# Kernel optimization log

Hardware: AMD Instinct MI355X
Metric: run time of the kernel (lower is better)

The kernel has to match this reference:

```python
import jax, jax.numpy as jnp
import numpy as np

L, D = 8192, 2048


def setup_inputs() -> dict:
    key = jax.random.key(0)
    kx, kA, kB, kC = jax.random.split(key, 4)
    x = jax.random.normal(kx, (L, D), dtype=jnp.float32)
    A = jax.random.normal(kA, (D,), dtype=jnp.float32)
    B = jax.random.normal(kB, (D,), dtype=jnp.float32)
    C = jax.random.normal(kC, (D,), dtype=jnp.float32)
    return {"x": x, "A": A, "B": B, "C": C}


def reference(x, A, B, C):
    # state_t = A * state_{t-1} + B * x_t ; y_t = tanh(C * state_t)
    Bx = B * x  # [L, D], precompute input injection

    def step(state, bx_t):
        state = A * state + bx_t
        return state, jnp.tanh(C * state)

    _, ys = jax.lax.scan(step, jnp.zeros((D,), dtype=x.dtype), Bx)
    return ys  # [L, D]
```

## Files before the change

kernel.cpp:

```cpp
#include <hip/hip_runtime.h>
#include <math.h>


#define LL 8192
#define DD 2048
#define CL 32
#define NC (LL / CL)
#define G4 (DD / 4)

typedef float f32x4 __attribute__((ext_vector_type(4)));

__device__ __forceinline__ float fast_tanh(float z)
{
    float e = __builtin_amdgcn_exp2f(z * 2.885390081777927f);
    return 1.0f - 2.0f * __builtin_amdgcn_rcpf(e + 1.0f);
}

__global__ __launch_bounds__(256) void mamba_p1(
    const float4* __restrict__ x4, const float4* __restrict__ A4,
    const float4* __restrict__ B4, float4* __restrict__ loc4)
{
    int lin   = blockIdx.x * 256 + threadIdx.x;
    int chunk = lin >> 9;
    int grp   = lin & (G4 - 1);

    float4 a = A4[grp];
    float4 b = B4[grp];
    float sx = 0.f, sy = 0.f, sz = 0.f, sw = 0.f;

    const float4* xp = x4 + (size_t)chunk * CL * G4 + grp;
    #pragma unroll
    for (int t0 = 0; t0 < CL; t0 += 16) {
        float4 v[16];
        #pragma unroll
        for (int k = 0; k < 16; ++k)
            v[k] = xp[(size_t)(t0 + k) * G4];
        #pragma unroll
        for (int k = 0; k < 16; ++k) {
            sx = fmaf(a.x, sx, b.x * v[k].x);
            sy = fmaf(a.y, sy, b.y * v[k].y);
            sz = fmaf(a.z, sz, b.z * v[k].z);
            sw = fmaf(a.w, sw, b.w * v[k].w);
        }
    }
    loc4[(size_t)chunk * G4 + grp] = make_float4(sx, sy, sz, sw);
}

__global__ __launch_bounds__(64) void mamba_p2(
    const float* __restrict__ A, const float* __restrict__ loc,
    float* __restrict__ car)
{
    int ch = blockIdx.x * 64 + threadIdx.x;
    float p = A[ch];
    #pragma unroll
    for (int i = 0; i < 5; ++i) p *= p;

    float c = 0.f;
    for (int c0 = 0; c0 < NC; c0 += 64) {
        float lv[64];
        #pragma unroll
        for (int k = 0; k < 64; ++k)
            lv[k] = loc[(size_t)(c0 + k) * DD + ch];
        #pragma unroll
        for (int k = 0; k < 64; ++k) {
            car[(size_t)(c0 + k) * DD + ch] = c;
            c = fmaf(p, c, lv[k]);
        }
    }
}

__global__ __launch_bounds__(256) void mamba_p3(
    const float4* __restrict__ x4, const float4* __restrict__ A4,
    const float4* __restrict__ B4, const float4* __restrict__ C4,
    const float4* __restrict__ car4, float4* __restrict__ y4)
{
    int lin   = blockIdx.x * 256 + threadIdx.x;
    int chunk = lin >> 9;
    int grp   = lin & (G4 - 1);

    float4 a = A4[grp];
    float4 b = B4[grp];
    float4 c = C4[grp];
    float4 s0 = car4[(size_t)chunk * G4 + grp];
    float sx = s0.x, sy = s0.y, sz = s0.z, sw = s0.w;

    const float4* xp = x4 + (size_t)chunk * CL * G4 + grp;
    float4*       yp = y4 + (size_t)chunk * CL * G4 + grp;

    #pragma unroll
    for (int t0 = 0; t0 < CL; t0 += 8) {
        float4 v[8];
        #pragma unroll
        for (int k = 0; k < 8; ++k)
            v[k] = xp[(size_t)(t0 + k) * G4];
        #pragma unroll
        for (int k = 0; k < 8; ++k) {
            sx = fmaf(a.x, sx, b.x * v[k].x);
            sy = fmaf(a.y, sy, b.y * v[k].y);
            sz = fmaf(a.z, sz, b.z * v[k].z);
            sw = fmaf(a.w, sw, b.w * v[k].w);
            f32x4 o;
            o.x = fast_tanh(c.x * sx);
            o.y = fast_tanh(c.y * sy);
            o.z = fast_tanh(c.z * sz);
            o.w = fast_tanh(c.w * sw);
            __builtin_nontemporal_store(o, (f32x4*)&yp[(size_t)(t0 + k) * G4]);
        }
    }
}

extern "C" void kernel_launch(void* const* d_in, const int* in_sizes, int n_in,
                              void* d_out, int out_size, void* d_ws, size_t ws_size,
                              hipStream_t stream)
{
    const float4* x4 = (const float4*)d_in[0];
    const float*  Af = (const float*)d_in[1];
    const float4* A4 = (const float4*)d_in[1];
    const float4* B4 = (const float4*)d_in[2];
    const float4* C4 = (const float4*)d_in[3];
    float4* y4 = (float4*)d_out;

    float*  locf = (float*)d_ws;
    float4* loc4 = (float4*)d_ws;
    float*  carf = locf + (size_t)NC * DD;
    float4* car4 = (float4*)carf;

    const int nthreads = NC * G4;
    mamba_p1<<<nthreads / 256, 256, 0, stream>>>(x4, A4, B4, loc4);
    mamba_p2<<<DD / 64, 64, 0, stream>>>(Af, locf, carf);
    mamba_p3<<<nthreads / 256, 256, 0, stream>>>(x4, A4, B4, C4, car4, y4);
}
```

Before: 48.57 us.

## Fuse carry-scan pass into chunk-reduce kernel via last-block atomic ticket

Merges the separate carry-propagation kernel into the first kernel. Each block takes an atomic ticket, the last four blocks spin until every block has finished and then do the sequential carry scan over chunks, each thread handling two channels. This removes one kernel launch and its gap, but adds a memset launch, a spin-wait, and a serial scan running on only four blocks (1024 threads). It also batches the tanh outputs in the third kernel before issuing the stores.

Result: slower. 74.34 us (+53.1%).

```diff
diff --git a/kernel.cpp b/kernel.cpp
--- a/kernel.cpp
+++ b/kernel.cpp
@@ -7,6 +7,8 @@
 #define CL 32
 #define NC (LL / CL)
 #define G4 (DD / 4)
+#define NBLK1 (NC * G4 / 256)
+#define NFIN 4
 
 typedef float f32x4 __attribute__((ext_vector_type(4)));
 
@@ -16,18 +18,19 @@
     return 1.0f - 2.0f * __builtin_amdgcn_rcpf(e + 1.0f);
 }
 
-__global__ __launch_bounds__(256) void mamba_p1(
+__global__ __launch_bounds__(256) void mamba_k1(
     const float4* __restrict__ x4, const float4* __restrict__ A4,
-    const float4* __restrict__ B4, float4* __restrict__ loc4)
+    const float4* __restrict__ B4, float4* __restrict__ loc4,
+    float* __restrict__ car, unsigned* __restrict__ cnt)
 {
-    int lin   = blockIdx.x * 256 + threadIdx.x;
-    int chunk = lin >> 9;
-    int grp   = lin & (G4 - 1);
+    const int lin   = blockIdx.x * 256 + threadIdx.x;
+    const int chunk = lin >> 9;
+    const int grp   = lin & (G4 - 1);
 
-    float4 a = A4[grp];
-    float4 b = B4[grp];
+    const float4 a = A4[grp];
+    const float4 b = B4[grp];
+
     float sx = 0.f, sy = 0.f, sz = 0.f, sw = 0.f;
-
     const float4* xp = x4 + (size_t)chunk * CL * G4 + grp;
     #pragma unroll
     for (int t0 = 0; t0 < CL; t0 += 16) {
@@ -44,27 +47,49 @@
         }
     }
     loc4[(size_t)chunk * G4 + grp] = make_float4(sx, sy, sz, sw);
-}
 
-__global__ __launch_bounds__(64) void mamba_p2(
-    const float* __restrict__ A, const float* __restrict__ loc,
-    float* __restrict__ car)
-{
-    int ch = blockIdx.x * 64 + threadIdx.x;
-    float p = A[ch];
+    __shared__ unsigned ticket_s;
+    __syncthreads();
+    if (threadIdx.x == 0) {
+        __threadfence();
+        ticket_s = __hip_atomic_fetch_add(&cnt[0], 1u,
+                       __ATOMIC_RELAXED, __HIP_MEMORY_SCOPE_AGENT);
+    }
+    __syncthreads();
+    const unsigned ticket = ticket_s;
+    if (ticket < NBLK1 - NFIN) return;
+
+    if (threadIdx.x == 0) {
+        while (__hip_atomic_load(&cnt[0], __ATOMIC_RELAXED,
+                                 __HIP_MEMORY_SCOPE_AGENT) < NBLK1)
+            __builtin_amdgcn_s_sleep(1);
+        __threadfence();
+    }
+    __syncthreads();
+
+    const int f  = (int)ticket - (NBLK1 - NFIN);
+    const int ch = f * 512 + (int)threadIdx.x * 2;
+
+    float pa = ((const float*)A4)[ch];
+    float pb = ((const float*)A4)[ch + 1];
     #pragma unroll
-    for (int i = 0; i < 5; ++i) p *= p;
+    for (int i = 0; i < 5; ++i) { pa *= pa; pb *= pb; }
 
-    float c = 0.f;
-    for (int c0 = 0; c0 < NC; c0 += 64) {
-        float lv[64];
+    const float2* locv = (const float2*)loc4;
+    float2*       carv = (float2*)car;
+    const int     colv = ch >> 1;
+
+    float cx = 0.f, cy = 0.f;
+    for (int j0 = 0; j0 < NC; j0 += 32) {
+        float2 lv[32];
         #pragma unroll
-        for (int k = 0; k < 64; ++k)
-            lv[k] = loc[(size_t)(c0 + k) * DD + ch];
+        for (int k = 0; k < 32; ++k)
+            lv[k] = locv[(size_t)(j0 + k) * (DD / 2) + colv];
         #pragma unroll
-        for (int k = 0; k < 64; ++k) {
-            car[(size_t)(c0 + k) * DD + ch] = c;
-            c = fmaf(p, c, lv[k]);
+        for (int k = 0; k < 32; ++k) {
+            carv[(size_t)(j0 + k) * (DD / 2) + colv] = make_float2(cx, cy);
+            cx = fmaf(pa, cx, lv[k].x);
+            cy = fmaf(pb, cy, lv[k].y);
         }
     }
 }
@@ -74,13 +99,13 @@
     const float4* __restrict__ B4, const float4* __restrict__ C4,
     const float4* __restrict__ car4, float4* __restrict__ y4)
 {
-    int lin   = blockIdx.x * 256 + threadIdx.x;
-    int chunk = lin >> 9;
-    int grp   = lin & (G4 - 1);
+    const int lin   = blockIdx.x * 256 + threadIdx.x;
+    const int chunk = lin >> 9;
+    const int grp   = lin & (G4 - 1);
 
-    float4 a = A4[grp];
-    float4 b = B4[grp];
-    float4 c = C4[grp];
+    const float4 a = A4[grp];
+    const float4 b = B4[grp];
+    const float4 c = C4[grp];
     float4 s0 = car4[(size_t)chunk * G4 + grp];
     float sx = s0.x, sy = s0.y, sz = s0.z, sw = s0.w;
 
@@ -93,19 +118,21 @@
         #pragma unroll
         for (int k = 0; k < 8; ++k)
             v[k] = xp[(size_t)(t0 + k) * G4];
+        f32x4 o[8];
         #pragma unroll
         for (int k = 0; k < 8; ++k) {
             sx = fmaf(a.x, sx, b.x * v[k].x);
             sy = fmaf(a.y, sy, b.y * v[k].y);
             sz = fmaf(a.z, sz, b.z * v[k].z);
             sw = fmaf(a.w, sw, b.w * v[k].w);
-            f32x4 o;
-            o.x = fast_tanh(c.x * sx);
-            o.y = fast_tanh(c.y * sy);
-            o.z = fast_tanh(c.z * sz);
-            o.w = fast_tanh(c.w * sw);
-            __builtin_nontemporal_store(o, (f32x4*)&yp[(size_t)(t0 + k) * G4]);
+            o[k].x = fast_tanh(c.x * sx);
+            o[k].y = fast_tanh(c.y * sy);
+            o[k].z = fast_tanh(c.z * sz);
+            o[k].w = fast_tanh(c.w * sw);
         }
+        #pragma unroll
+        for (int k = 0; k < 8; ++k)
+            __builtin_nontemporal_store(o[k], (f32x4*)&yp[(size_t)(t0 + k) * G4]);
     }
 }
 
@@ -114,19 +141,18 @@
                               hipStream_t stream)
 {
     const float4* x4 = (const float4*)d_in[0];
-    const float*  Af = (const float*)d_in[1];
     const float4* A4 = (const float4*)d_in[1];
     const float4* B4 = (const float4*)d_in[2];
     const float4* C4 = (const float4*)d_in[3];
     float4* y4 = (float4*)d_out;
 
-    float*  locf = (float*)d_ws;
     float4* loc4 = (float4*)d_ws;
-    float*  carf = locf + (size_t)NC * DD;
+    float*  carf = (float*)d_ws + (size_t)NC * DD;
     float4* car4 = (float4*)carf;
+    unsigned* cnt = (unsigned*)((char*)d_ws + (size_t)NC * DD * 4 * 2);
 
-    const int nthreads = NC * G4;
-    mamba_p1<<<nthreads / 256, 256, 0, stream>>>(x4, A4, B4, loc4);
-    mamba_p2<<<DD / 64, 64, 0, stream>>>(Af, locf, carf);
-    mamba_p3<<<nthreads / 256, 256, 0, stream>>>(x4, A4, B4, C4, car4, y4);
+    (void)hipMemsetAsync(cnt, 0, 16, stream);
+
+    mamba_k1<<<NBLK1, 256, 0, stream>>>(x4, A4, B4, loc4, carf, cnt);
+    mamba_p3<<<NBLK1, 256, 0, stream>>>(x4, A4, B4, C4, car4, y4);
 }
```
